# Optimization experiments

Measured on AMD Instinct MI355X. Metric: run time of the kernel, lower is better.

The kernel has to match this reference:

```python
import jax, jax.numpy as jnp
import numpy as np

ALPHA_MIN = 1e-6
SN_EPS = 1e-6


def _spectral_normalize(W, u):
    # One power iteration (torch spectral_norm, n_power_iterations=1).
    v = W.T @ u
    v = v / (jnp.linalg.norm(v) + SN_EPS)
    u1 = W @ v
    u1 = u1 / (jnp.linalg.norm(u1) + SN_EPS)
    u1 = jax.lax.stop_gradient(u1)
    v = jax.lax.stop_gradient(v)
    sigma = u1 @ (W @ v)
    return W / sigma


def setup_inputs() -> dict:
    key = jax.random.key(0)
    ks = jax.random.split(key, 11)
    B, T, D, K = 32, 2048, 512, 128
    x = jax.random.normal(ks[0], (B, T, D), jnp.float32)
    dt = jax.random.uniform(ks[1], (B, T), jnp.float32)
    alpha_mod = jax.random.normal(ks[2], (B, T, K), jnp.float32)
    omega_mod = jax.random.normal(ks[3], (B, T, K), jnp.float32)
    tau_mod = jax.random.normal(ks[4], (B, T, 1), jnp.float32)
    s_real_raw = jax.random.normal(ks[5], (K,), jnp.float32)
    s_imag = jax.random.normal(ks[6], (K,), jnp.float32)
    tau_raw = jax.random.normal(ks[7], (1,), jnp.float32)
    W_orig = jax.random.normal(ks[8], (K, D), jnp.float32) * (1.0 / np.sqrt(D))
    b = jax.random.normal(ks[9], (K,), jnp.float32) * 0.01
    u_sn = jax.random.normal(ks[10], (K,), jnp.float32)
    u_sn = u_sn / jnp.linalg.norm(u_sn)
    return {"x": x, "dt": dt, "alpha_mod": alpha_mod, "omega_mod": omega_mod,
            "tau_mod": tau_mod, "s_real_raw": s_real_raw, "s_imag": s_imag,
            "tau_raw": tau_raw, "W_orig": W_orig, "b": b, "u_sn": u_sn}


def reference(x, dt, alpha_mod, omega_mod, tau_mod, s_real_raw, s_imag,
              tau_raw, W_orig, b, u_sn):
    B, T, D = x.shape
    K = W_orig.shape[0]

    # global timescale and poles
    tau = jax.nn.softplus(tau_raw[0]) + 1e-3
    alpha0 = (jax.nn.softplus(s_real_raw) + ALPHA_MIN) * tau  # [K]
    omega0 = s_imag * tau                                      # [K]

    # time-varying modulation (all log-scale)
    scale = jnp.exp(tau_mod)                                   # [B,T,1]
    alpha = alpha0 * jnp.exp(alpha_mod) * scale                # [B,T,K]
    omega = omega0 * jnp.exp(omega_mod) * scale                # [B,T,K]

    dt3 = dt[..., None]                                        # [B,T,1]
    rho = jnp.exp(-alpha * dt3)                                # [B,T,K]
    theta = omega * dt3
    cos_t = jnp.cos(theta)
    sin_t = jnp.sin(theta)

    # spectral-norm projection u = x @ W_sn^T + b -> [B,T,K]
    W_sn = _spectral_normalize(W_orig, u_sn)
    u = jnp.einsum('btd,kd->btk', x, W_sn) + b

    # complex recurrence: z_t = rho_t * e^{i theta_t} * z_{t-1} + u_t
    def step(carry, inp):
        c, s = carry
        rt, ct, st, ut = inp
        c_new = rt * (c * ct - s * st) + ut
        s_new = rt * (c * st + s * ct)
        return (c_new, s_new), (c_new, s_new)

    xs = (jnp.swapaxes(rho, 0, 1), jnp.swapaxes(cos_t, 0, 1),
          jnp.swapaxes(sin_t, 0, 1), jnp.swapaxes(u, 0, 1))  # [T,B,K]
    init = (jnp.zeros((B, K), u.dtype), jnp.zeros((B, K), u.dtype))
    _, (C, S) = jax.lax.scan(step, init, xs)
    C = jnp.swapaxes(C, 0, 1)  # [B,T,K]
    S = jnp.swapaxes(S, 0, 1)
    return jnp.concatenate([C, S], axis=-1)  # [B,T,2K]
```

## Files before the change

kernel.cpp:

```cpp
#include <hip/hip_runtime.h>
#include <hip/hip_bf16.h>
#include <math.h>

typedef __bf16 bf16x8 __attribute__((ext_vector_type(8)));
typedef __bf16 bf16x4 __attribute__((ext_vector_type(4)));
typedef __bf16 bf16x2 __attribute__((ext_vector_type(2)));
typedef float f32x4 __attribute__((ext_vector_type(4)));

#define B_SZ 32
#define T_SZ 2048
#define D_SZ 512
#define K_SZ 128
#define TC 32
#define NC 64

__device__ __forceinline__ float softplus_f(float x){
  return x > 20.f ? x : log1pf(expf(x));
}

__global__ __launch_bounds__(512) void sn_prep(const float* __restrict__ W,
                                               const float* __restrict__ u_sn,
                                               __bf16* __restrict__ Wb){
  __shared__ float red[512];
  __shared__ float vsh[512];
  __shared__ float ush[128];
  const int t = threadIdx.x;
  if (t < 128) ush[t] = u_sn[t];
  __syncthreads();
  float t1 = 0.f;
  #pragma unroll 8
  for (int k = 0; k < K_SZ; ++k) t1 += W[k*D_SZ + t] * ush[k];
  red[t] = t1 * t1;
  __syncthreads();
  for (int s = 256; s > 0; s >>= 1){ if (t < s) red[t] += red[t+s]; __syncthreads(); }
  const float n1 = sqrtf(red[0]);
  vsh[t] = t1 / (n1 + 1e-6f);
  __syncthreads();
  float t2 = 0.f;
  if (t < 128){
    const float4* Wr = (const float4*)(W + (size_t)t * D_SZ);
    const float4* vp = (const float4*)vsh;
    #pragma unroll 8
    for (int d = 0; d < D_SZ/4; ++d){
      const float4 a = Wr[d], v = vp[d];
      t2 += a.x*v.x + a.y*v.y + a.z*v.z + a.w*v.w;
    }
  }
  __syncthreads();
  red[t] = (t < 128) ? t2*t2 : 0.f;
  __syncthreads();
  for (int s = 256; s > 0; s >>= 1){ if (t < s) red[t] += red[t+s]; __syncthreads(); }
  const float n2sq = red[0];
  const float sigma = n2sq / (sqrtf(n2sq) + 1e-6f);
  const float inv = 1.f / sigma;
  for (int i = t; i < K_SZ*D_SZ/4; i += 512){
    const float4 v = ((const float4*)W)[i];
    bf16x4 o; o[0]=(__bf16)(v.x*inv); o[1]=(__bf16)(v.y*inv);
    o[2]=(__bf16)(v.z*inv); o[3]=(__bf16)(v.w*inv);
    ((bf16x4*)Wb)[i] = o;
  }
}

__global__ __launch_bounds__(256) void gemm_xw(const float* __restrict__ X,
                                               const __bf16* __restrict__ Wb,
                                               __bf16* __restrict__ U){
  __shared__ bf16x8 As[1024];
  __shared__ bf16x8 Bs[1024];
  const int tid = threadIdx.x;
  const int lane = tid & 63;
  const int wid = tid >> 6;
  const int wm = wid >> 1, wn = wid & 1;
  const int rowbase = blockIdx.x * 128;
  const int L15 = lane & 15, Lq = lane >> 4;
  f32x4 acc[4][4] = {};

  for (int kk = 0; kk < D_SZ; kk += 64){
    #pragma unroll
    for (int r = 0; r < 4; ++r){
      const int fc = tid + 256*r;
      const int row = fc >> 3, cg = fc & 7;
      const float4* p = (const float4*)(X + (size_t)(rowbase + row)*D_SZ + kk + cg*8);
      const float4 v0 = p[0], v1 = p[1];
      bf16x8 f;
      f[0]=(__bf16)v0.x; f[1]=(__bf16)v0.y; f[2]=(__bf16)v0.z; f[3]=(__bf16)v0.w;
      f[4]=(__bf16)v1.x; f[5]=(__bf16)v1.y; f[6]=(__bf16)v1.z; f[7]=(__bf16)v1.w;
      const int fb = ((row >> 4) << 1) | (cg >> 2);
      const int ll = (row & 15) | ((cg & 3) << 4);
      As[fb*64 + ll] = f;
      Bs[fb*64 + ll] = *(const bf16x8*)(Wb + (size_t)row*D_SZ + kk + cg*8);
    }
    __syncthreads();
    #pragma unroll
    for (int s = 0; s < 2; ++s){
      bf16x8 af[4], bfr[4];
      #pragma unroll
      for (int ii = 0; ii < 4; ++ii) af[ii]  = As[((wm*4+ii)*2 + s)*64 + lane];
      #pragma unroll
      for (int jj = 0; jj < 4; ++jj) bfr[jj] = Bs[((wn*4+jj)*2 + s)*64 + lane];
      #pragma unroll
      for (int ii = 0; ii < 4; ++ii)
        #pragma unroll
        for (int jj = 0; jj < 4; ++jj)
          acc[ii][jj] = __builtin_amdgcn_mfma_f32_16x16x32_bf16(af[ii], bfr[jj], acc[ii][jj], 0, 0, 0);
    }
    __syncthreads();
  }
  #pragma unroll
  for (int ii = 0; ii < 4; ++ii){
    const int m = rowbase + (wm*4+ii)*16 + (Lq << 2);
    #pragma unroll
    for (int jj = 0; jj < 4; ++jj){
      const int n = (wn*4+jj)*16 + L15;
      #pragma unroll
      for (int r = 0; r < 4; ++r)
        U[(size_t)(m + r)*K_SZ + n] = (__bf16)acc[ii][jj][r];
    }
  }
}

__global__ __launch_bounds__(256) void pass_a(
    const float* __restrict__ alpha_mod, const float* __restrict__ omega_mod,
    const __bf16* __restrict__ Uarr, const float* __restrict__ dt,
    const float* __restrict__ tau_mod, const float* __restrict__ s_real,
    const float* __restrict__ s_imag, const float* __restrict__ tau_raw,
    const float* __restrict__ bvec,
    float2* __restrict__ sumA, float2* __restrict__ sumT,
    float2* __restrict__ Zr, float2* __restrict__ Zi){
  const int t = threadIdx.x;
  const int kh = t & 63;
  const int cl = t >> 6;
  const int b = blockIdx.y;
  const int c = blockIdx.x*4 + cl;
  const int t0 = c * TC;
  __shared__ float sdt[4*TC], ssc[4*TC];
  if (t < 128){
    const int tg = blockIdx.x*4*TC + t;
    sdt[t] = dt[b*T_SZ + tg];
    ssc[t] = __expf(tau_mod[b*T_SZ + tg]);
  }
  __syncthreads();
  const float tau = softplus_f(tau_raw[0]) + 1e-3f;
  const float2 sr = ((const float2*)s_real)[kh];
  const float2 si = ((const float2*)s_imag)[kh];
  const float2 bk = ((const float2*)bvec)[kh];
  const float a0[2] = {(softplus_f(sr.x)+1e-6f)*tau, (softplus_f(sr.y)+1e-6f)*tau};
  const float w0[2] = {si.x*tau, si.y*tau};
  float zr[2]={0,0}, zs[2]={0,0}, sA[2]={0,0}, sT[2]={0,0};
  const float* sd = sdt + cl*TC;
  const float* ss = ssc + cl*TC;
  const size_t row = (size_t)(b*T_SZ + t0);
  const float2* amp = (const float2*)(alpha_mod + row*K_SZ) + kh;
  const float2* omp = (const float2*)(omega_mod + row*K_SZ) + kh;
  const bf16x2* up  = (const bf16x2*)(Uarr + row*K_SZ) + kh;
  #pragma unroll 4
  for (int i = 0; i < TC; ++i){
    const float2 am = amp[(size_t)i*64];
    const float2 om = omp[(size_t)i*64];
    const bf16x2 u2 = up[(size_t)i*64];
    const float scdt = ss[i] * sd[i];
    #pragma unroll
    for (int j = 0; j < 2; ++j){
      const float ad = a0[j] * __expf(j ? am.y : am.x) * scdt;
      const float th = w0[j] * __expf(j ? om.y : om.x) * scdt;
      const float rho = __expf(-ad);
      float st, ct; __sincosf(th, &st, &ct);
      const float uu = (float)u2[j] + (j ? bk.y : bk.x);
      const float nr = rho*(zr[j]*ct - zs[j]*st) + uu;
      const float ns = rho*(zr[j]*st + zs[j]*ct);
      zr[j] = nr; zs[j] = ns;
      sA[j] += ad; sT[j] += th;
    }
  }
  const size_t idx = ((size_t)(b*NC + c))*64 + kh;
  sumA[idx] = make_float2(sA[0], sA[1]);
  sumT[idx] = make_float2(sT[0], sT[1]);
  Zr[idx]   = make_float2(zr[0], zr[1]);
  Zi[idx]   = make_float2(zs[0], zs[1]);
}

__global__ __launch_bounds__(256) void pass_b(
    const float2* __restrict__ sumA, const float2* __restrict__ sumT,
    const float2* __restrict__ Zr, const float2* __restrict__ Zi,
    float2* __restrict__ Cr, float2* __restrict__ Ci){
  const int id = blockIdx.x*256 + threadIdx.x;
  const int b = id >> 6, kh = id & 63;
  float er[2]={0,0}, ei[2]={0,0};
  #pragma unroll 4
  for (int c = 0; c < NC; ++c){
    const size_t idx = ((size_t)(b*NC + c))*64 + kh;
    Cr[idx] = make_float2(er[0], er[1]);
    Ci[idx] = make_float2(ei[0], ei[1]);
    const float2 sa = sumA[idx], st4 = sumT[idx];
    const float2 zr = Zr[idx],   zi  = Zi[idx];
    #pragma unroll
    for (int j = 0; j < 2; ++j){
      const float rho = __expf(-(j ? sa.y : sa.x));
      float st, ct; __sincosf(j ? st4.y : st4.x, &st, &ct);
      const float ar = rho*ct, ai = rho*st;
      const float zrj = j ? zr.y : zr.x, zij = j ? zi.y : zi.x;
      const float nr = zrj + ar*er[j] - ai*ei[j];
      const float ni = zij + ar*ei[j] + ai*er[j];
      er[j] = nr; ei[j] = ni;
    }
  }
}

__global__ __launch_bounds__(256) void pass_c(
    const float* __restrict__ alpha_mod, const float* __restrict__ omega_mod,
    const __bf16* __restrict__ Uarr, const float* __restrict__ dt,
    const float* __restrict__ tau_mod, const float* __restrict__ s_real,
    const float* __restrict__ s_imag, const float* __restrict__ tau_raw,
    const float* __restrict__ bvec,
    const float2* __restrict__ Cr, const float2* __restrict__ Ci,
    float* __restrict__ out){
  const int t = threadIdx.x;
  const int kh = t & 63;
  const int cl = t >> 6;
  const int b = blockIdx.y;
  const int c = blockIdx.x*4 + cl;
  const int t0 = c * TC;
  __shared__ float sdt[4*TC], ssc[4*TC];
  if (t < 128){
    const int tg = blockIdx.x*4*TC + t;
    sdt[t] = dt[b*T_SZ + tg];
    ssc[t] = __expf(tau_mod[b*T_SZ + tg]);
  }
  __syncthreads();
  const float tau = softplus_f(tau_raw[0]) + 1e-3f;
  const float2 sr = ((const float2*)s_real)[kh];
  const float2 si = ((const float2*)s_imag)[kh];
  const float2 bk = ((const float2*)bvec)[kh];
  const float a0[2] = {(softplus_f(sr.x)+1e-6f)*tau, (softplus_f(sr.y)+1e-6f)*tau};
  const float w0[2] = {si.x*tau, si.y*tau};
  const size_t cidx = ((size_t)(b*NC + c))*64 + kh;
  const float2 cr = Cr[cidx], cim = Ci[cidx];
  float zr[2] = {cr.x, cr.y}, zs[2] = {cim.x, cim.y};
  const float* sd = sdt + cl*TC;
  const float* ss = ssc + cl*TC;
  const size_t row = (size_t)(b*T_SZ + t0);
  const float2* amp = (const float2*)(alpha_mod + row*K_SZ) + kh;
  const float2* omp = (const float2*)(omega_mod + row*K_SZ) + kh;
  const bf16x2* up  = (const bf16x2*)(Uarr + row*K_SZ) + kh;
  float2* outC = (float2*)(out + row*(2*K_SZ)) + kh;
  float2* outS = outC + 64;
  #pragma unroll 4
  for (int i = 0; i < TC; ++i){
    const float2 am = amp[(size_t)i*64];
    const float2 om = omp[(size_t)i*64];
    const bf16x2 u2 = up[(size_t)i*64];
    const float scdt = ss[i] * sd[i];
    #pragma unroll
    for (int j = 0; j < 2; ++j){
      const float ad = a0[j] * __expf(j ? am.y : am.x) * scdt;
      const float th = w0[j] * __expf(j ? om.y : om.x) * scdt;
      const float rho = __expf(-ad);
      float st, ct; __sincosf(th, &st, &ct);
      const float uu = (float)u2[j] + (j ? bk.y : bk.x);
      const float nr = rho*(zr[j]*ct - zs[j]*st) + uu;
      const float ns = rho*(zr[j]*st + zs[j]*ct);
      zr[j] = nr; zs[j] = ns;
    }
    outC[(size_t)i*128] = make_float2(zr[0], zr[1]);
    outS[(size_t)i*128] = make_float2(zs[0], zs[1]);
  }
}

extern "C" void kernel_launch(void* const* d_in, const int* in_sizes, int n_in,
                              void* d_out, int out_size, void* d_ws, size_t ws_size,
                              hipStream_t stream){
  (void)in_sizes; (void)n_in; (void)out_size; (void)ws_size;
  const float* x         = (const float*)d_in[0];
  const float* dt        = (const float*)d_in[1];
  const float* alpha_mod = (const float*)d_in[2];
  const float* omega_mod = (const float*)d_in[3];
  const float* tau_mod   = (const float*)d_in[4];
  const float* s_real    = (const float*)d_in[5];
  const float* s_imag    = (const float*)d_in[6];
  const float* tau_raw   = (const float*)d_in[7];
  const float* W         = (const float*)d_in[8];
  const float* bvec      = (const float*)d_in[9];
  const float* u_sn      = (const float*)d_in[10];
  float* out = (float*)d_out;

  char* w = (char*)d_ws;
  __bf16* Wb = (__bf16*)w;
  __bf16* U  = (__bf16*)(w + 131072);
  size_t off = 131072 + (size_t)B_SZ*T_SZ*K_SZ*2;
  const size_t SUMN = (size_t)B_SZ*NC*K_SZ*4;
  float2* sumA = (float2*)(w + off); off += SUMN;
  float2* sumT = (float2*)(w + off); off += SUMN;
  float2* Zr   = (float2*)(w + off); off += SUMN;
  float2* Zi   = (float2*)(w + off); off += SUMN;
  float2* Cr   = (float2*)(w + off); off += SUMN;
  float2* Ci   = (float2*)(w + off); off += SUMN;

  sn_prep<<<1, 512, 0, stream>>>(W, u_sn, Wb);
  gemm_xw<<<(B_SZ*T_SZ)/128, 256, 0, stream>>>(x, Wb, U);
  pass_a<<<dim3(NC/4, B_SZ), 256, 0, stream>>>(alpha_mod, omega_mod, U, dt, tau_mod,
                                               s_real, s_imag, tau_raw, bvec,
                                               sumA, sumT, Zr, Zi);
  pass_b<<<8, 256, 0, stream>>>(sumA, sumT, Zr, Zi, Cr, Ci);
  pass_c<<<dim3(NC/4, B_SZ), 256, 0, stream>>>(alpha_mod, omega_mod, U, dt, tau_mod,
                                               s_real, s_imag, tau_raw, bvec,
                                               Cr, Ci, out);
}
```

Baseline: 340.0 us.

## Double-buffer GEMM shared tiles with register prefetch and XOR swizzle

The x·W projection GEMM now prefetches the next K-slice of X and W into registers while MFMAs run on the current slice. Shared memory is double-buffered, which removes the trailing barrier per iteration. An XOR swizzle on the LDS index is added to cut bank conflicts on stores and fragment loads. In exchange the kernel uses more LDS and registers, which may lower occupancy.

```diff
diff --git a/kernel.cpp b/kernel.cpp
--- a/kernel.cpp
+++ b/kernel.cpp
@@ -64,8 +64,8 @@
 __global__ __launch_bounds__(256) void gemm_xw(const float* __restrict__ X,
                                                const __bf16* __restrict__ Wb,
                                                __bf16* __restrict__ U){
-  __shared__ bf16x8 As[1024];
-  __shared__ bf16x8 Bs[1024];
+  __shared__ bf16x8 As[2][1024];
+  __shared__ bf16x8 Bs[2][1024];
   const int tid = threadIdx.x;
   const int lane = tid & 63;
   const int wid = tid >> 6;
@@ -74,36 +74,69 @@
   const int L15 = lane & 15, Lq = lane >> 4;
   f32x4 acc[4][4] = {};
 
+  const int rowA = tid >> 3;
+  const int cg   = tid & 7;
+  const int colo = cg * 8;
+  int pidx[4];
+  #pragma unroll
+  for (int r = 0; r < 4; ++r){
+    const int row = rowA + 32*r;
+    const int fb = ((row >> 4) << 1) | (cg >> 2);
+    const int ll = (row & 15) | ((cg & 3) << 4);
+    pidx[r] = (fb*64 + ll) ^ cg;
+  }
+  const float* Xb  = X  + (size_t)(rowbase + rowA)*D_SZ + colo;
+  const __bf16* Bb = Wb + (size_t)rowA*D_SZ + colo;
+
+  float4 va[4], vb[4];
+  bf16x8 wreg[4];
+  #pragma unroll
+  for (int r = 0; r < 4; ++r){
+    const float4* q = (const float4*)(Xb + (size_t)(32*r)*D_SZ);
+    va[r] = q[0]; vb[r] = q[1];
+    wreg[r] = *(const bf16x8*)(Bb + (size_t)(32*r)*D_SZ);
+  }
+
+  int pb = 0;
   for (int kk = 0; kk < D_SZ; kk += 64){
     #pragma unroll
     for (int r = 0; r < 4; ++r){
-      const int fc = tid + 256*r;
-      const int row = fc >> 3, cg = fc & 7;
-      const float4* p = (const float4*)(X + (size_t)(rowbase + row)*D_SZ + kk + cg*8);
-      const float4 v0 = p[0], v1 = p[1];
       bf16x8 f;
-      f[0]=(__bf16)v0.x; f[1]=(__bf16)v0.y; f[2]=(__bf16)v0.z; f[3]=(__bf16)v0.w;
-      f[4]=(__bf16)v1.x; f[5]=(__bf16)v1.y; f[6]=(__bf16)v1.z; f[7]=(__bf16)v1.w;
-      const int fb = ((row >> 4) << 1) | (cg >> 2);
-      const int ll = (row & 15) | ((cg & 3) << 4);
-      As[fb*64 + ll] = f;
-      Bs[fb*64 + ll] = *(const bf16x8*)(Wb + (size_t)row*D_SZ + kk + cg*8);
+      f[0]=(__bf16)va[r].x; f[1]=(__bf16)va[r].y; f[2]=(__bf16)va[r].z; f[3]=(__bf16)va[r].w;
+      f[4]=(__bf16)vb[r].x; f[5]=(__bf16)vb[r].y; f[6]=(__bf16)vb[r].z; f[7]=(__bf16)vb[r].w;
+      As[pb][pidx[r]] = f;
+      Bs[pb][pidx[r]] = wreg[r];
     }
     __syncthreads();
+    if (kk + 64 < D_SZ){
+      #pragma unroll
+      for (int r = 0; r < 4; ++r){
+        const float4* q = (const float4*)(Xb + (size_t)(32*r)*D_SZ + kk + 64);
+        va[r] = q[0]; vb[r] = q[1];
+        wreg[r] = *(const bf16x8*)(Bb + (size_t)(32*r)*D_SZ + kk + 64);
+      }
+    }
     #pragma unroll
     for (int s = 0; s < 2; ++s){
       bf16x8 af[4], bfr[4];
-      #pragma unroll
-      for (int ii = 0; ii < 4; ++ii) af[ii]  = As[((wm*4+ii)*2 + s)*64 + lane];
-      #pragma unroll
-      for (int jj = 0; jj < 4; ++jj) bfr[jj] = Bs[((wn*4+jj)*2 + s)*64 + lane];
+      const int swz = (s << 2) | (lane >> 4);
+      #pragma unroll
+      for (int ii = 0; ii < 4; ++ii){
+        const int fb = ((wm*4+ii) << 1) | s;
+        af[ii] = As[pb][(fb*64 + lane) ^ swz];
+      }
+      #pragma unroll
+      for (int jj = 0; jj < 4; ++jj){
+        const int fb = ((wn*4+jj) << 1) | s;
+        bfr[jj] = Bs[pb][(fb*64 + lane) ^ swz];
+      }
       #pragma unroll
       for (int ii = 0; ii < 4; ++ii)
         #pragma unroll
         for (int jj = 0; jj < 4; ++jj)
           acc[ii][jj] = __builtin_amdgcn_mfma_f32_16x16x32_bf16(af[ii], bfr[jj], acc[ii][jj], 0, 0, 0);
     }
-    __syncthreads();
+    pb ^= 1;
   }
   #pragma unroll
   for (int ii = 0; ii < 4; ++ii){
```

Measured after the change: 335.3 us. About the same (-1.4%).
